# Kernel tuning notes

Hardware: AMD Instinct MI355X
Metric: run time of the kernel (lower is better)

The kernel has to match this reference:

```python
import jax, jax.numpy as jnp
import numpy as np

D_MODEL = 768
NUM_HEADS = 12
HEAD_DIM = D_MODEL // NUM_HEADS
B, T = 2, 4096


def setup_inputs() -> dict:
    key = jax.random.key(0)
    k1, k2, k3, k4, k5 = jax.random.split(key, 5)
    s_in = 1.0 / np.sqrt(D_MODEL)
    return {
        "x": jax.random.normal(k1, (B, T, D_MODEL), dtype=jnp.float32),
        "w_qkv": jax.random.normal(k2, (3 * D_MODEL, D_MODEL), dtype=jnp.float32) * s_in,
        "b_qkv": jax.random.normal(k3, (3 * D_MODEL,), dtype=jnp.float32) * 0.01,
        "w_out": jax.random.normal(k4, (D_MODEL, D_MODEL), dtype=jnp.float32) * s_in,
        "b_out": jax.random.normal(k5, (D_MODEL,), dtype=jnp.float32) * 0.01,
    }


def reference(x, w_qkv, b_qkv, w_out, b_out):
    b, t, c = x.shape
    # qkv: [B,T,3C] -> [3,B,H,T,Dh]  (torch Linear: x @ W.T + b)
    qkv = (x @ w_qkv.T + b_qkv).reshape(b, t, 3, NUM_HEADS, HEAD_DIM)
    qkv = jnp.transpose(qkv, (2, 0, 3, 1, 4))
    q, k, v = qkv[0], qkv[1], qkv[2]
    scale = 1.0 / np.sqrt(HEAD_DIM)
    scores = jnp.einsum("bhqd,bhkd->bhqk", q, k) * scale  # [B,H,T,T]
    causal = jnp.tril(jnp.ones((t, t), dtype=bool))
    scores = jnp.where(causal, scores, -jnp.inf)
    weights = jax.nn.softmax(scores, axis=-1)
    out = jnp.einsum("bhqk,bhkd->bhqd", weights, v)  # [B,H,T,Dh]
    out = jnp.transpose(out, (0, 2, 1, 3)).reshape(b, t, c)
    return out @ w_out.T + b_out
```

## Files before the change

### kernel.cpp

```cpp
#include <hip/hip_runtime.h>


#define NHEADS 12
#define DHEAD  64
#define TSEQ   4096
#define BATCH  2
#define CMODEL 768
#define MTOT   (BATCH * TSEQ)
#define NQKV   (3 * CMODEL)
#define NBH    (BATCH * NHEADS)

typedef __attribute__((ext_vector_type(8))) short s16x8;
typedef __attribute__((ext_vector_type(4))) float f32x4;
typedef __attribute__((ext_vector_type(4))) unsigned short u16x4;
typedef __attribute__((ext_vector_type(2))) unsigned int u32x2;

__device__ __forceinline__ unsigned short f2bf(float f) {
    unsigned u = __builtin_bit_cast(unsigned, f);
    u += 0x7fffu + ((u >> 16) & 1u);
    return (unsigned short)(u >> 16);
}

__device__ __forceinline__ unsigned pk2bf(float a, float b) {
    return (unsigned)f2bf(a) | ((unsigned)f2bf(b) << 16);
}

__device__ __forceinline__ unsigned cvtpk(float lo, float hi) {
    unsigned r;
    asm("v_cvt_pk_bf16_f32 %0, %1, %2" : "=v"(r) : "v"(lo), "v"(hi));
    return r;
}

__device__ __forceinline__ float fexp2(float x) {
    return __builtin_amdgcn_exp2f(x);
}

__device__ __forceinline__ void async_load16(const void* g, void* l) {
    __builtin_amdgcn_global_load_lds(
        (const __attribute__((address_space(1))) unsigned*)g,
        (__attribute__((address_space(3))) unsigned*)l, 16, 0, 0);
}

__global__ __launch_bounds__(256) void cvt3_kernel(
    const float* __restrict__ s0, const float* __restrict__ s1,
    const float* __restrict__ s2,
    unsigned short* __restrict__ d0, unsigned short* __restrict__ d1,
    unsigned short* __restrict__ d2, int n0, int n1, int n2)
{
    int i = blockIdx.x * 256 + threadIdx.x;
    const float* s; unsigned short* d; int j;
    if (i < n0)                { s = s0; d = d0; j = i; }
    else if (i < n0 + n1)      { s = s1; d = d1; j = i - n0; }
    else if (i < n0 + n1 + n2) { s = s2; d = d2; j = i - n0 - n1; }
    else return;
    f32x4 v = ((const f32x4*)s)[j];
    u32x2 o;
    o.x = pk2bf(v.x, v.y);
    o.y = pk2bf(v.z, v.w);
    ((u32x2*)d)[j] = o;
}

__global__ __launch_bounds__(256) void gemm_qkv_kernel(
    const unsigned short* __restrict__ A,
    const unsigned short* __restrict__ Bw,
    const float* __restrict__ bias,
    unsigned short* __restrict__ Qb,
    unsigned short* __restrict__ Kb,
    unsigned short* __restrict__ Vt)
{
    __shared__ unsigned short sA[128][64];
    __shared__ unsigned short sB[128][64];
    const int n0 = blockIdx.x * 128;
    const int m0 = blockIdx.y * 128;
    const int tid = threadIdx.x;
    const int l = tid & 63, g = l >> 4, l15 = l & 15;
    const int w = tid >> 6, wm = w & 1, wn = w >> 1;
    const int wbase = tid & 192;
    const int seg = n0 / 768;

    f32x4 acc[4][4];
#pragma unroll
    for (int a = 0; a < 4; a++)
#pragma unroll
        for (int b = 0; b < 4; b++) acc[a][b] = (f32x4){0.f, 0.f, 0.f, 0.f};

    if (seg < 2) {
        for (int k0 = 0; k0 < 768; k0 += 64) {
#pragma unroll
            for (int i = 0; i < 4; i++) {
                const int idx = i * 256 + tid;
                const int row = idx >> 3, pc = idx & 7;
                const int lc = pc ^ (row & 7);
                async_load16(&A[(size_t)(m0 + row) * 768 + k0 + lc * 8],
                             &sA[0][0] + (size_t)(i * 256 + wbase) * 8);
                async_load16(&Bw[(size_t)(n0 + row) * 768 + k0 + lc * 8],
                             &sB[0][0] + (size_t)(i * 256 + wbase) * 8);
            }
            __syncthreads();
#pragma unroll
            for (int ks = 0; ks < 2; ks++) {
                const int cc = ((ks * 4 + g) ^ (l15 & 7)) * 8;
                s16x8 af[4], bf[4];
#pragma unroll
                for (int mt = 0; mt < 4; mt++)
                    af[mt] = *(const s16x8*)&sA[wm * 64 + mt * 16 + l15][cc];
#pragma unroll
                for (int nt = 0; nt < 4; nt++)
                    bf[nt] = *(const s16x8*)&sB[wn * 64 + nt * 16 + l15][cc];
#pragma unroll
                for (int nt = 0; nt < 4; nt++)
#pragma unroll
                    for (int mt = 0; mt < 4; mt++)
                        acc[nt][mt] = __builtin_amdgcn_mfma_f32_16x16x32_bf16(
                            bf[nt], af[mt], acc[nt][mt], 0, 0, 0);
            }
            __syncthreads();
        }

        unsigned short* dst = (seg == 0) ? Qb : Kb;
        const float sc = (seg == 0) ? 0.18033688011f : 1.0f;
        const int hh = ((n0 - seg * 768) + wn * 64) >> 6;
#pragma unroll
        for (int nt = 0; nt < 4; nt++) {
            const int dh = nt * 16 + g * 4;
            const f32x4 bv4 = *(const f32x4*)&bias[n0 + wn * 64 + dh];
#pragma unroll
            for (int mt = 0; mt < 4; mt++) {
                const int m = m0 + wm * 64 + mt * 16 + l15;
                const int b = m >> 12, t = m & 4095;
                u32x2 pk;
                pk.x = pk2bf((acc[nt][mt][0] + bv4[0]) * sc,
                             (acc[nt][mt][1] + bv4[1]) * sc);
                pk.y = pk2bf((acc[nt][mt][2] + bv4[2]) * sc,
                             (acc[nt][mt][3] + bv4[3]) * sc);
                *(u32x2*)&dst[(((size_t)(b * NHEADS + hh) * TSEQ + t) << 6) + dh] = pk;
            }
        }
    } else {
        for (int k0 = 0; k0 < 768; k0 += 64) {
#pragma unroll
            for (int i = 0; i < 4; i++) {
                const int idx = i * 256 + tid;
                const int row = idx >> 3, pc = idx & 7;
                const int lc = pc ^ (row & 7);
                async_load16(&A[(size_t)(m0 + row) * 768 + k0 + lc * 8],
                             &sA[0][0] + (size_t)(i * 256 + wbase) * 8);
                async_load16(&Bw[(size_t)(n0 + row) * 768 + k0 + lc * 8],
                             &sB[0][0] + (size_t)(i * 256 + wbase) * 8);
            }
            __syncthreads();
#pragma unroll
            for (int ks = 0; ks < 2; ks++) {
                const int cc = ((ks * 4 + g) ^ (l15 & 7)) * 8;
                s16x8 af[4], bf[4];
#pragma unroll
                for (int mt = 0; mt < 4; mt++)
                    af[mt] = *(const s16x8*)&sA[wm * 64 + mt * 16 + l15][cc];
#pragma unroll
                for (int nt = 0; nt < 4; nt++)
                    bf[nt] = *(const s16x8*)&sB[wn * 64 + nt * 16 + l15][cc];
#pragma unroll
                for (int mt = 0; mt < 4; mt++)
#pragma unroll
                    for (int nt = 0; nt < 4; nt++)
                        acc[mt][nt] = __builtin_amdgcn_mfma_f32_16x16x32_bf16(
                            af[mt], bf[nt], acc[mt][nt], 0, 0, 0);
            }
            __syncthreads();
        }

#pragma unroll
        for (int nt = 0; nt < 4; nt++) {
            const int n = n0 + wn * 64 + nt * 16 + l15;
            const float bv = bias[n];
            const int hh = (n - 1536) >> 6;
            const int dh = n & 63;
#pragma unroll
            for (int mt = 0; mt < 4; mt++) {
                const int mg = m0 + wm * 64 + mt * 16 + g * 4;
                const int b = mg >> 12, t = mg & 4095;
                u32x2 pk;
                pk.x = pk2bf(acc[mt][nt][0] + bv, acc[mt][nt][1] + bv);
                pk.y = pk2bf(acc[mt][nt][2] + bv, acc[mt][nt][3] + bv);
                *(u32x2*)&Vt[((size_t)(b * NHEADS + hh) * DHEAD + dh) * TSEQ + t] = pk;
            }
        }
    }
}

__device__ __forceinline__ void process_tile(
    const unsigned short (&sKb)[64][64],
    const unsigned short (&sVb)[64][64],
    unsigned short (&sPTw)[2][16][64],
    const s16x8 (&qa)[2][2],
    f32x4 (&o)[2][4], f32x4 (&lac)[2],
    s16x8 vones, int kt, int qg0, bool mask, int g, int l15)
{
    const int xk = l15 & 7;
    const int qg1 = qg0 + 16;

    f32x4 st[2][4];
#pragma unroll
    for (int nt = 0; nt < 4; nt++) {
        st[0][nt] = (f32x4){0.f, 0.f, 0.f, 0.f};
        st[1][nt] = (f32x4){0.f, 0.f, 0.f, 0.f};
    }
    __builtin_amdgcn_s_setprio(1);
#pragma unroll
    for (int ks = 0; ks < 2; ks++) {
        const int cc = ((ks * 4 + g) ^ xk) * 8;
#pragma unroll
        for (int nt = 0; nt < 4; nt++) {
            const s16x8 akf = *(const s16x8*)&sKb[nt * 16 + l15][cc];
            st[0][nt] = __builtin_amdgcn_mfma_f32_16x16x32_bf16(
                akf, qa[0][ks], st[0][nt], 0, 0, 0);
            st[1][nt] = __builtin_amdgcn_mfma_f32_16x16x32_bf16(
                akf, qa[1][ks], st[1][nt], 0, 0, 0);
        }
    }
    __builtin_amdgcn_s_setprio(0);

    if (mask) {
#pragma unroll
        for (int nt = 0; nt < 4; nt++)
#pragma unroll
            for (int r = 0; r < 4; r++) {
                const int key = kt + nt * 16 + g * 4 + r;
                if (key > qg0) st[0][nt][r] = -1e30f;
                if (key > qg1) st[1][nt][r] = -1e30f;
            }
    }

#pragma unroll
    for (int qf = 0; qf < 2; qf++) {
#pragma unroll
        for (int nt = 0; nt < 4; nt++) {
            float p0 = fexp2(st[qf][nt][0]);
            float p1 = fexp2(st[qf][nt][1]);
            float p2 = fexp2(st[qf][nt][2]);
            float p3 = fexp2(st[qf][nt][3]);
            u32x2 pk;
            pk.x = cvtpk(p0, p1);
            pk.y = cvtpk(p2, p3);
            const int phys = ((nt * 2 + (g >> 1)) ^ xk) * 8 + (g & 1) * 4;
            *(u32x2*)&sPTw[qf][l15][phys] = pk;
        }
    }

    __builtin_amdgcn_s_setprio(1);
#pragma unroll
    for (int ks = 0; ks < 2; ks++) {
        const int cc = ((ks * 4 + g) ^ xk) * 8;
        const s16x8 bp0 = *(const s16x8*)&sPTw[0][l15][cc];
        const s16x8 bp1 = *(const s16x8*)&sPTw[1][l15][cc];
#pragma unroll
        for (int nt = 0; nt < 4; nt++) {
            const s16x8 avf = *(const s16x8*)&sVb[nt * 16 + l15][cc];
            o[0][nt] = __builtin_amdgcn_mfma_f32_16x16x32_bf16(
                avf, bp0, o[0][nt], 0, 0, 0);
            o[1][nt] = __builtin_amdgcn_mfma_f32_16x16x32_bf16(
                avf, bp1, o[1][nt], 0, 0, 0);
        }
        lac[0] = __builtin_amdgcn_mfma_f32_16x16x32_bf16(vones, bp0, lac[0], 0, 0, 0);
        lac[1] = __builtin_amdgcn_mfma_f32_16x16x32_bf16(vones, bp1, lac[1], 0, 0, 0);
    }
    __builtin_amdgcn_s_setprio(0);
}

__global__ __launch_bounds__(256, 3) void attn_kernel(
    const unsigned short* __restrict__ Qb,
    const unsigned short* __restrict__ Kb,
    const unsigned short* __restrict__ Vt,
    unsigned short* __restrict__ Ob,
    float* __restrict__ oPart,
    float* __restrict__ lPart)
{
    __shared__ unsigned short sK[2][64][64];
    __shared__ unsigned short sV[2][64][64];
    __shared__ unsigned short sPT[4][2][16][64];
    const int bh   = blockIdx.x;
    const int p    = blockIdx.y >> 1;
    const int half = blockIdx.y & 1;
    const int jA = p, jB = 31 - p;
    const int nA = 2 * p + 2;
    const int aCount = (half == 0) ? nA : 0;
    const int bStart = (half == 0) ? 0 : (31 - 2 * p);
    const int bCount = 33 - aCount;
    const int tid = threadIdx.x;
    const int w = tid >> 6, l = tid & 63, g = l >> 4, l15 = l & 15;
    const int wbase = tid & 192;

    const int rl0 = w * 32 + l15;
    const int b = bh / NHEADS, hd = bh - b * NHEADS;

    s16x8 vones;
#pragma unroll
    for (int e = 0; e < 8; e++) vones[e] = (short)0x3F80;

    const unsigned short* Kbase = Kb + (size_t)bh * TSEQ * DHEAD;
    const unsigned short* Vbase = Vt + (size_t)bh * DHEAD * TSEQ;

    auto stage = [&](int jt, int buf) {
        const int kt = jt * 64;
#pragma unroll
        for (int pp = 0; pp < 2; pp++) {
            const int idx = pp * 256 + tid;
            const int row = idx >> 3, pc = idx & 7;
            const int lc = pc ^ (row & 7);
            async_load16(&Kbase[(size_t)(kt + row) * DHEAD + lc * 8],
                         &sK[buf][0][0] + (size_t)(pp * 256 + wbase) * 8);
            async_load16(&Vbase[(size_t)row * TSEQ + kt + lc * 8],
                         &sV[buf][0][0] + (size_t)(pp * 256 + wbase) * 8);
        }
    };

    stage((half == 0) ? 0 : bStart, 0);
    __syncthreads();

    if (half == 0) {
        const int qg0A = jA * 128 + rl0;
        const unsigned short* QpA = Qb + ((size_t)bh * TSEQ + qg0A) * DHEAD;
        s16x8 qA[2][2];
        qA[0][0] = *(const s16x8*)&QpA[g * 8];
        qA[0][1] = *(const s16x8*)&QpA[32 + g * 8];
        qA[1][0] = *(const s16x8*)&QpA[16 * DHEAD + g * 8];
        qA[1][1] = *(const s16x8*)&QpA[16 * DHEAD + 32 + g * 8];

        f32x4 oA[2][4];
        f32x4 lacA[2];
#pragma unroll
        for (int nt = 0; nt < 4; nt++) {
            oA[0][nt] = (f32x4){0.f, 0.f, 0.f, 0.f};
            oA[1][nt] = (f32x4){0.f, 0.f, 0.f, 0.f};
        }
        lacA[0] = (f32x4){0.f, 0.f, 0.f, 0.f};
        lacA[1] = (f32x4){0.f, 0.f, 0.f, 0.f};

        for (int s = 0; s < nA; s++) {
            const int buf = s & 1;
            if (s + 1 < nA) stage(s + 1, buf ^ 1);
            else stage(0, buf ^ 1);
            process_tile(sK[buf], sV[buf], sPT[w], qA, oA, lacA, vones,
                         s * 64, qg0A, s >= nA - 2, g, l15);
            __syncthreads();
        }

#pragma unroll
        for (int qf = 0; qf < 2; qf++) {
            const int qg = qg0A + qf * 16;
            const float inv = 1.0f / lacA[qf][0];
#pragma unroll
            for (int nt = 0; nt < 4; nt++) {
                u32x2 pk;
                pk.x = pk2bf(oA[qf][nt][0] * inv, oA[qf][nt][1] * inv);
                pk.y = pk2bf(oA[qf][nt][2] * inv, oA[qf][nt][3] * inv);
                *(u32x2*)&Ob[((size_t)b * TSEQ + qg) * CMODEL + hd * DHEAD +
                             nt * 16 + g * 4] = pk;
            }
        }
    }

    {
        const int qg0B = jB * 128 + rl0;
        const unsigned short* QpB = Qb + ((size_t)bh * TSEQ + qg0B) * DHEAD;
        s16x8 qB[2][2];
        qB[0][0] = *(const s16x8*)&QpB[g * 8];
        qB[0][1] = *(const s16x8*)&QpB[32 + g * 8];
        qB[1][0] = *(const s16x8*)&QpB[16 * DHEAD + g * 8];
        qB[1][1] = *(const s16x8*)&QpB[16 * DHEAD + 32 + g * 8];

        f32x4 oB[2][4];
        f32x4 lacB[2];
#pragma unroll
        for (int nt = 0; nt < 4; nt++) {
            oB[0][nt] = (f32x4){0.f, 0.f, 0.f, 0.f};
            oB[1][nt] = (f32x4){0.f, 0.f, 0.f, 0.f};
        }
        lacB[0] = (f32x4){0.f, 0.f, 0.f, 0.f};
        lacB[1] = (f32x4){0.f, 0.f, 0.f, 0.f};

        for (int s = 0; s < bCount; s++) {
            const int buf = (aCount + s) & 1;
            if (s + 1 < bCount) stage(bStart + s + 1, buf ^ 1);
            const bool mask = (half == 1) && (s >= 31);
            process_tile(sK[buf], sV[buf], sPT[w], qB, oB, lacB, vones,
                         (bStart + s) * 64, qg0B, mask, g, l15);
            __syncthreads();
        }

        const int pairIdx = bh * 16 + p;
        const size_t slot = (size_t)pairIdx * 2 + half;
        float* oS = oPart + slot * (128 * 64);
        float* lS = lPart + slot * 128;
#pragma unroll
        for (int qf = 0; qf < 2; qf++) {
            const int rl = rl0 + qf * 16;
#pragma unroll
            for (int nt = 0; nt < 4; nt++)
                *(f32x4*)&oS[(size_t)rl * 64 + nt * 16 + g * 4] = oB[qf][nt];
            if (g == 0) lS[rl] = lacB[qf][0];
        }
    }
}

__global__ __launch_bounds__(256) void combine_kernel(
    const float* __restrict__ oPart,
    const float* __restrict__ lPart,
    unsigned short* __restrict__ Ob)
{
    const int i = blockIdx.x * 256 + threadIdx.x;
    const int c4 = i & 15;
    const int rl = (i >> 4) & 127;
    const int p  = (i >> 11) & 15;
    const int bh = i >> 15;
    const int pair = bh * 16 + p;
    const float* o0 = oPart + ((size_t)pair * 2 + 0) * (128 * 64);
    const float* o1 = oPart + ((size_t)pair * 2 + 1) * (128 * 64);
    const float l0 = lPart[((size_t)pair * 2 + 0) * 128 + rl];
    const float l1 = lPart[((size_t)pair * 2 + 1) * 128 + rl];
    const float inv = 1.0f / (l0 + l1);
    const f32x4 a = *(const f32x4*)&o0[(size_t)rl * 64 + c4 * 4];
    const f32x4 c = *(const f32x4*)&o1[(size_t)rl * 64 + c4 * 4];
    const int b = bh / NHEADS, h = bh - b * NHEADS;
    const int qg = (31 - p) * 128 + rl;
    u32x2 pk;
    pk.x = pk2bf((a[0] + c[0]) * inv, (a[1] + c[1]) * inv);
    pk.y = pk2bf((a[2] + c[2]) * inv, (a[3] + c[3]) * inv);
    *(u32x2*)&Ob[((size_t)b * TSEQ + qg) * CMODEL + h * DHEAD + c4 * 4] = pk;
}

__global__ __launch_bounds__(256) void gemm_out_kernel(
    const unsigned short* __restrict__ A,
    const unsigned short* __restrict__ Bw,
    const float* __restrict__ bias,
    float* __restrict__ out)
{
    __shared__ unsigned short sA[128][64];
    __shared__ unsigned short sB[128][64];
    const int n0 = blockIdx.x * 128;
    const int m0 = blockIdx.y * 128;
    const int tid = threadIdx.x;
    const int l = tid & 63, g = l >> 4, l15 = l & 15;
    const int w = tid >> 6, wm = w & 1, wn = w >> 1;
    const int wbase = tid & 192;

    f32x4 acc[4][4];
#pragma unroll
    for (int mt = 0; mt < 4; mt++)
#pragma unroll
        for (int nt = 0; nt < 4; nt++) acc[mt][nt] = (f32x4){0.f, 0.f, 0.f, 0.f};

    for (int k0 = 0; k0 < 768; k0 += 64) {
#pragma unroll
        for (int i = 0; i < 4; i++) {
            const int idx = i * 256 + tid;
            const int row = idx >> 3, pc = idx & 7;
            const int lc = pc ^ (row & 7);
            async_load16(&A[(size_t)(m0 + row) * 768 + k0 + lc * 8],
                         &sA[0][0] + (size_t)(i * 256 + wbase) * 8);
            async_load16(&Bw[(size_t)(n0 + row) * 768 + k0 + lc * 8],
                         &sB[0][0] + (size_t)(i * 256 + wbase) * 8);
        }
        __syncthreads();
#pragma unroll
        for (int ks = 0; ks < 2; ks++) {
            const int cc = ((ks * 4 + g) ^ (l15 & 7)) * 8;
            s16x8 af[4], bf[4];
#pragma unroll
            for (int mt = 0; mt < 4; mt++)
                af[mt] = *(const s16x8*)&sA[wm * 64 + mt * 16 + l15][cc];
#pragma unroll
            for (int nt = 0; nt < 4; nt++)
                bf[nt] = *(const s16x8*)&sB[wn * 64 + nt * 16 + l15][cc];
#pragma unroll
            for (int mt = 0; mt < 4; mt++)
#pragma unroll
                for (int nt = 0; nt < 4; nt++)
                    acc[mt][nt] = __builtin_amdgcn_mfma_f32_16x16x32_bf16(
                        af[mt], bf[nt], acc[mt][nt], 0, 0, 0);
        }
        __syncthreads();
    }

#pragma unroll
    for (int nt = 0; nt < 4; nt++) {
        const int n = n0 + wn * 64 + nt * 16 + l15;
        const float bv = bias[n];
#pragma unroll
        for (int mt = 0; mt < 4; mt++)
#pragma unroll
            for (int r = 0; r < 4; r++) {
                const int m = m0 + wm * 64 + mt * 16 + g * 4 + r;
                out[(size_t)m * CMODEL + n] = acc[mt][nt][r] + bv;
            }
    }
}

extern "C" void kernel_launch(void* const* d_in, const int* in_sizes, int n_in,
                              void* d_out, int out_size, void* d_ws, size_t ws_size,
                              hipStream_t stream) {
    const float* x     = (const float*)d_in[0];
    const float* w_qkv = (const float*)d_in[1];
    const float* b_qkv = (const float*)d_in[2];
    const float* w_out = (const float*)d_in[3];
    const float* b_out = (const float*)d_in[4];
    float* out = (float*)d_out;

    char* ws = (char*)d_ws;
    size_t off = 0;
    auto alloc = [&](size_t bytes) -> void* {
        void* p = (void*)(ws + off);
        off += (bytes + 255) & ~(size_t)255;
        return p;
    };
    unsigned short* xb    = (unsigned short*)alloc((size_t)MTOT * CMODEL * 2);
    unsigned short* wqkvb = (unsigned short*)alloc((size_t)NQKV * CMODEL * 2);
    unsigned short* woutb = (unsigned short*)alloc((size_t)CMODEL * CMODEL * 2);
    unsigned short* Qb    = (unsigned short*)alloc((size_t)NBH * TSEQ * DHEAD * 2);
    unsigned short* Kb    = (unsigned short*)alloc((size_t)NBH * TSEQ * DHEAD * 2);
    unsigned short* Vt    = (unsigned short*)alloc((size_t)NBH * TSEQ * DHEAD * 2);
    unsigned short* Ob    = (unsigned short*)alloc((size_t)MTOT * CMODEL * 2);
    float* oPart = (float*)alloc((size_t)NBH * 16 * 2 * 128 * 64 * 4);
    float* lPart = (float*)alloc((size_t)NBH * 16 * 2 * 128 * 4);

    const int n40 = MTOT * CMODEL / 4;
    const int n41 = NQKV * CMODEL / 4;
    const int n42 = CMODEL * CMODEL / 4;
    const int nblk = (n40 + n41 + n42 + 255) / 256;
    cvt3_kernel<<<dim3(nblk), 256, 0, stream>>>(
        x, w_qkv, w_out, xb, wqkvb, woutb, n40, n41, n42);

    gemm_qkv_kernel<<<dim3(NQKV / 128, MTOT / 128), 256, 0, stream>>>(
        xb, wqkvb, b_qkv, Qb, Kb, Vt);
    attn_kernel<<<dim3(NBH, 32), 256, 0, stream>>>(
        Qb, Kb, Vt, Ob, oPart, lPart);
    combine_kernel<<<dim3(NBH * 16 * 128 * 16 / 256), 256, 0, stream>>>(
        oPart, lPart, Ob);
    gemm_out_kernel<<<dim3(CMODEL / 128, MTOT / 128), 256, 0, stream>>>(
        Ob, woutb, b_out, out);
}
```

Measured before the change: 230.0 us.

## Double-buffer output GEMM with 128x64 tiles and relax attention loop barriers

```diff
diff --git a/kernel.cpp b/kernel.cpp
--- a/kernel.cpp
+++ b/kernel.cpp
@@ -39,6 +39,12 @@
     __builtin_amdgcn_global_load_lds(
         (const __attribute__((address_space(1))) unsigned*)g,
         (__attribute__((address_space(3))) unsigned*)l, 16, 0, 0);
+}
+
+__device__ __forceinline__ void raw_barrier() {
+    __builtin_amdgcn_sched_barrier(0);
+    __builtin_amdgcn_s_barrier();
+    __builtin_amdgcn_sched_barrier(0);
 }
 
 __global__ __launch_bounds__(256) void cvt3_kernel(
@@ -340,9 +346,10 @@
             const int buf = s & 1;
             if (s + 1 < nA) stage(s + 1, buf ^ 1);
             else stage(0, buf ^ 1);
+            asm volatile("s_waitcnt vmcnt(4)" ::: "memory");
             process_tile(sK[buf], sV[buf], sPT[w], qA, oA, lacA, vones,
                          s * 64, qg0A, s >= nA - 2, g, l15);
-            __syncthreads();
+            raw_barrier();
         }
 
 #pragma unroll
@@ -381,11 +388,16 @@
 
         for (int s = 0; s < bCount; s++) {
             const int buf = (aCount + s) & 1;
-            if (s + 1 < bCount) stage(bStart + s + 1, buf ^ 1);
+            if (s + 1 < bCount) {
+                stage(bStart + s + 1, buf ^ 1);
+                asm volatile("s_waitcnt vmcnt(4)" ::: "memory");
+            } else {
+                asm volatile("s_waitcnt vmcnt(0)" ::: "memory");
+            }
             const bool mask = (half == 1) && (s >= 31);
             process_tile(sK[buf], sV[buf], sPT[w], qB, oB, lacB, vones,
                          (bStart + s) * 64, qg0B, mask, g, l15);
-            __syncthreads();
+            raw_barrier();
         }
 
         const int pairIdx = bh * 16 + p;
@@ -435,64 +447,85 @@
     const float* __restrict__ bias,
     float* __restrict__ out)
 {
-    __shared__ unsigned short sA[128][64];
-    __shared__ unsigned short sB[128][64];
-    const int n0 = blockIdx.x * 128;
+    __shared__ unsigned short sA[2][128][64];
+    __shared__ unsigned short sB[2][64][64];
+    const int n0 = blockIdx.x * 64;
     const int m0 = blockIdx.y * 128;
     const int tid = threadIdx.x;
     const int l = tid & 63, g = l >> 4, l15 = l & 15;
     const int w = tid >> 6, wm = w & 1, wn = w >> 1;
     const int wbase = tid & 192;
 
-    f32x4 acc[4][4];
-#pragma unroll
-    for (int mt = 0; mt < 4; mt++)
-#pragma unroll
-        for (int nt = 0; nt < 4; nt++) acc[mt][nt] = (f32x4){0.f, 0.f, 0.f, 0.f};
-
-    for (int k0 = 0; k0 < 768; k0 += 64) {
+    auto stage = [&](int k0, int buf) {
 #pragma unroll
         for (int i = 0; i < 4; i++) {
             const int idx = i * 256 + tid;
             const int row = idx >> 3, pc = idx & 7;
             const int lc = pc ^ (row & 7);
             async_load16(&A[(size_t)(m0 + row) * 768 + k0 + lc * 8],
-                         &sA[0][0] + (size_t)(i * 256 + wbase) * 8);
+                         &sA[buf][0][0] + (size_t)(i * 256 + wbase) * 8);
+        }
+#pragma unroll
+        for (int i = 0; i < 2; i++) {
+            const int idx = i * 256 + tid;
+            const int row = idx >> 3, pc = idx & 7;
+            const int lc = pc ^ (row & 7);
             async_load16(&Bw[(size_t)(n0 + row) * 768 + k0 + lc * 8],
-                         &sB[0][0] + (size_t)(i * 256 + wbase) * 8);
-        }
-        __syncthreads();
+                         &sB[buf][0][0] + (size_t)(i * 256 + wbase) * 8);
+        }
+    };
+
+    f32x4 acc[2][4];
+#pragma unroll
+    for (int nt = 0; nt < 2; nt++)
+#pragma unroll
+        for (int mt = 0; mt < 4; mt++) acc[nt][mt] = (f32x4){0.f, 0.f, 0.f, 0.f};
+
+    stage(0, 0);
+    __syncthreads();
+
+    for (int t = 0; t < 12; t++) {
+        const int buf = t & 1;
+        if (t + 1 < 12) {
+            stage((t + 1) * 64, buf ^ 1);
+            asm volatile("s_waitcnt vmcnt(6)" ::: "memory");
+        } else {
+            asm volatile("s_waitcnt vmcnt(0)" ::: "memory");
+        }
 #pragma unroll
         for (int ks = 0; ks < 2; ks++) {
             const int cc = ((ks * 4 + g) ^ (l15 & 7)) * 8;
-            s16x8 af[4], bf[4];
+            s16x8 af[4], bf2[2];
 #pragma unroll
             for (int mt = 0; mt < 4; mt++)
-                af[mt] = *(const s16x8*)&sA[wm * 64 + mt * 16 + l15][cc];
-#pragma unroll
-            for (int nt = 0; nt < 4; nt++)
-                bf[nt] = *(const s16x8*)&sB[wn * 64 + nt * 16 + l15][cc];
-#pragma unroll
-            for (int mt = 0; mt < 4; mt++)
-#pragma unroll
-                for (int nt = 0; nt < 4; nt++)
-                    acc[mt][nt] = __builtin_amdgcn_mfma_f32_16x16x32_bf16(
-                        af[mt], bf[nt], acc[mt][nt], 0, 0, 0);
-        }
-        __syncthreads();
-    }
-
-#pragma unroll
-    for (int nt = 0; nt < 4; nt++) {
-        const int n = n0 + wn * 64 + nt * 16 + l15;
-        const float bv = bias[n];
-#pragma unroll
-        for (int mt = 0; mt < 4; mt++)
-#pragma unroll
-            for (int r = 0; r < 4; r++) {
-                const int m = m0 + wm * 64 + mt * 16 + g * 4 + r;
-                out[(size_t)m * CMODEL + n] = acc[mt][nt][r] + bv;
-            }
+                af[mt] = *(const s16x8*)&sA[buf][wm * 64 + mt * 16 + l15][cc];
+#pragma unroll
+            for (int nt = 0; nt < 2; nt++)
+                bf2[nt] = *(const s16x8*)&sB[buf][wn * 32 + nt * 16 + l15][cc];
+#pragma unroll
+            for (int nt = 0; nt < 2; nt++)
+#pragma unroll
+                for (int mt = 0; mt < 4; mt++)
+                    acc[nt][mt] = __builtin_amdgcn_mfma_f32_16x16x32_bf16(
+                        bf2[nt], af[mt], acc[nt][mt], 0, 0, 0);
+        }
+        raw_barrier();
+    }
+
+#pragma unroll
+    for (int nt = 0; nt < 2; nt++) {
+        const int nb = n0 + wn * 32 + nt * 16 + g * 4;
+        const f32x4 bv4 = *(const f32x4*)&bias[nb];
+#pragma unroll
+        for (int mt = 0; mt < 4; mt++) {
+            const int m = m0 + wm * 64 + mt * 16 + l15;
+            f32x4 v;
+            v[0] = acc[nt][mt][0] + bv4[0];
+            v[1] = acc[nt][mt][1] + bv4[1];
+            v[2] = acc[nt][mt][2] + bv4[2];
+            v[3] = acc[nt][mt][3] + bv4[3];
+            *(f32x4*)&out[(size_t)m * CMODEL + nb] = v;
+        }
     }
 }
 
@@ -536,6 +569,6 @@
         Qb, Kb, Vt, Ob, oPart, lPart);
     combine_kernel<<<dim3(NBH * 16 * 128 * 16 / 256), 256, 0, stream>>>(
         oPart, lPart, Ob);
-    gemm_out_kernel<<<dim3(CMODEL / 128, MTOT / 128), 256, 0, stream>>>(
+    gemm_out_kernel<<<dim3(CMODEL / 64, MTOT / 128), 256, 0, stream>>>(
         Ob, woutb, b_out, out);
 }
```

Result: no change. 232.6 us (+1.1%).

## Remap GEMM blocks across XCDs and relax attention loop barriers

Applied to the files above, without the earlier changes.

```diff
diff --git a/kernel.cpp b/kernel.cpp
--- a/kernel.cpp
+++ b/kernel.cpp
@@ -39,6 +39,12 @@
     __builtin_amdgcn_global_load_lds(
         (const __attribute__((address_space(1))) unsigned*)g,
         (__attribute__((address_space(3))) unsigned*)l, 16, 0, 0);
+}
+
+__device__ __forceinline__ void raw_barrier() {
+    __builtin_amdgcn_sched_barrier(0);
+    __builtin_amdgcn_s_barrier();
+    __builtin_amdgcn_sched_barrier(0);
 }
 
 __global__ __launch_bounds__(256) void cvt3_kernel(
@@ -70,8 +76,10 @@
 {
     __shared__ unsigned short sA[128][64];
     __shared__ unsigned short sB[128][64];
-    const int n0 = blockIdx.x * 128;
-    const int m0 = blockIdx.y * 128;
+    const int idx = blockIdx.x + blockIdx.y * 18;
+    const int lid = (idx & 7) * 144 + (idx >> 3);
+    const int n0 = (lid % 18) * 128;
+    const int m0 = (lid / 18) * 128;
     const int tid = threadIdx.x;
     const int l = tid & 63, g = l >> 4, l15 = l & 15;
     const int w = tid >> 6, wm = w & 1, wn = w >> 1;
@@ -88,8 +96,8 @@
         for (int k0 = 0; k0 < 768; k0 += 64) {
 #pragma unroll
             for (int i = 0; i < 4; i++) {
-                const int idx = i * 256 + tid;
-                const int row = idx >> 3, pc = idx & 7;
+                const int idx2 = i * 256 + tid;
+                const int row = idx2 >> 3, pc = idx2 & 7;
                 const int lc = pc ^ (row & 7);
                 async_load16(&A[(size_t)(m0 + row) * 768 + k0 + lc * 8],
                              &sA[0][0] + (size_t)(i * 256 + wbase) * 8);
@@ -140,8 +148,8 @@
         for (int k0 = 0; k0 < 768; k0 += 64) {
 #pragma unroll
             for (int i = 0; i < 4; i++) {
-                const int idx = i * 256 + tid;
-                const int row = idx >> 3, pc = idx & 7;
+                const int idx2 = i * 256 + tid;
+                const int row = idx2 >> 3, pc = idx2 & 7;
                 const int lc = pc ^ (row & 7);
                 async_load16(&A[(size_t)(m0 + row) * 768 + k0 + lc * 8],
                              &sA[0][0] + (size_t)(i * 256 + wbase) * 8);
@@ -340,9 +348,10 @@
             const int buf = s & 1;
             if (s + 1 < nA) stage(s + 1, buf ^ 1);
             else stage(0, buf ^ 1);
+            asm volatile("s_waitcnt vmcnt(4)" ::: "memory");
             process_tile(sK[buf], sV[buf], sPT[w], qA, oA, lacA, vones,
                          s * 64, qg0A, s >= nA - 2, g, l15);
-            __syncthreads();
+            raw_barrier();
         }
 
 #pragma unroll
@@ -381,11 +390,16 @@
 
         for (int s = 0; s < bCount; s++) {
             const int buf = (aCount + s) & 1;
-            if (s + 1 < bCount) stage(bStart + s + 1, buf ^ 1);
+            if (s + 1 < bCount) {
+                stage(bStart + s + 1, buf ^ 1);
+                asm volatile("s_waitcnt vmcnt(4)" ::: "memory");
+            } else {
+                asm volatile("s_waitcnt vmcnt(0)" ::: "memory");
+            }
             const bool mask = (half == 1) && (s >= 31);
             process_tile(sK[buf], sV[buf], sPT[w], qB, oB, lacB, vones,
                          (bStart + s) * 64, qg0B, mask, g, l15);
-            __syncthreads();
+            raw_barrier();
         }
 
         const int pairIdx = bh * 16 + p;
@@ -437,8 +451,10 @@
 {
     __shared__ unsigned short sA[128][64];
     __shared__ unsigned short sB[128][64];
-    const int n0 = blockIdx.x * 128;
-    const int m0 = blockIdx.y * 128;
+    const int idx = blockIdx.x + blockIdx.y * 6;
+    const int lid = (idx & 7) * 48 + (idx >> 3);
+    const int n0 = (lid % 6) * 128;
+    const int m0 = (lid / 6) * 128;
     const int tid = threadIdx.x;
     const int l = tid & 63, g = l >> 4, l15 = l & 15;
     const int w = tid >> 6, wm = w & 1, wn = w >> 1;
@@ -453,8 +469,8 @@
     for (int k0 = 0; k0 < 768; k0 += 64) {
 #pragma unroll
         for (int i = 0; i < 4; i++) {
-            const int idx = i * 256 + tid;
-            const int row = idx >> 3, pc = idx & 7;
+            const int idx2 = i * 256 + tid;
+            const int row = idx2 >> 3, pc = idx2 & 7;
             const int lc = pc ^ (row & 7);
             async_load16(&A[(size_t)(m0 + row) * 768 + k0 + lc * 8],
                          &sA[0][0] + (size_t)(i * 256 + wbase) * 8);
```

After: 228.5 us. No clear change (-0.6%).
